# Kernel optimization log

Hardware: AMD Instinct MI355X
Metric: run time of the kernel (lower is better)

The kernel has to match this reference:

```python
import jax, jax.numpy as jnp
import numpy as np

N = 500000   # active voxels
CIN = 32
COUT = 64
K = 27       # 3x3x3 kernel taps
G = 8        # group norm groups
EPS = 1e-5


def group_norm(x, gamma, beta, num_groups=G, eps=EPS):
    # fvnn GroupNorm on sparse features with batch size 1: normalize each
    # channel-group over all active voxels (spatial) and channels in group.
    n, c = x.shape
    xg = x.reshape(n, num_groups, c // num_groups)
    mean = xg.mean(axis=(0, 2), keepdims=True)
    var = xg.var(axis=(0, 2), keepdims=True)
    xn = ((xg - mean) * jax.lax.rsqrt(var + eps)).reshape(n, c)
    return xn * gamma + beta


def sparse_conv(x, nbr_idx, W):
    # gather-based sparse 3x3x3 conv: W is [K, Cin, Cout]; loop over the 27
    # fixed kernel taps to avoid materializing the full [N, K, Cin] gather.
    out = jnp.zeros((x.shape[0], W.shape[2]), x.dtype)
    for k in range(W.shape[0]):
        out = out + jnp.take(x, nbr_idx[:, k], axis=0) @ W[k]
    return out


def setup_inputs() -> dict:
    key = jax.random.key(0)
    ks = jax.random.split(key, 8)
    s1 = 1.0 / np.sqrt(K * CIN)
    s2 = 1.0 / np.sqrt(K * COUT)
    return {
        "x": jax.random.normal(ks[0], (N, CIN), jnp.float32),
        "nbr_idx": jax.random.randint(ks[1], (N, K), 0, N, jnp.int32),
        "gamma1": jnp.ones((CIN,), jnp.float32),
        "beta1": jnp.zeros((CIN,), jnp.float32),
        "W1": jax.random.normal(ks[2], (K, CIN, COUT), jnp.float32) * s1,
        "gamma2": jnp.ones((COUT,), jnp.float32),
        "beta2": jnp.zeros((COUT,), jnp.float32),
        "W2": jax.random.normal(ks[3], (K, COUT, COUT), jnp.float32) * s2,
        "Wskip": jax.random.normal(ks[4], (CIN, COUT), jnp.float32) * (1.0 / np.sqrt(CIN)),
        "bskip": jnp.zeros((COUT,), jnp.float32),
        "feat_depth": 0,
    }


def reference(x, nbr_idx, gamma1, beta1, W1, gamma2, beta2, W2, Wskip, bskip, feat_depth):
    # decoder SparseResBlock, order 'gcs': GN -> SparseConv(bias=False) -> SiLU
    h = jax.nn.silu(sparse_conv(group_norm(x, gamma1, beta1), nbr_idx, W1))
    h = jax.nn.silu(sparse_conv(group_norm(h, gamma2, beta2), nbr_idx, W2))
    skip = x @ Wskip + bskip  # 1x1 sparse conv == per-voxel linear
    return (h + skip, feat_depth)
```

## Files before the change

### kernel.cpp

```cpp
#include <hip/hip_runtime.h>
#include <hip/hip_bf16.h>

typedef __bf16 bf16x8 __attribute__((ext_vector_type(8)));
typedef __bf16 bf16x4 __attribute__((ext_vector_type(4)));
typedef float  f32x4  __attribute__((ext_vector_type(4)));

#define MFMA16(a, b, c) __builtin_amdgcn_mfma_f32_16x16x32_bf16((a), (b), (c), 0, 0, 0)

__global__ void zero_stats_kernel(float* s) { s[threadIdx.x] = 0.0f; }

__global__ __launch_bounds__(256) void caststats_kernel(
    const float4* __restrict__ x, bf16x4* __restrict__ xb,
    float* __restrict__ stats, int nvec)
{
    int nth = gridDim.x * blockDim.x;
    int gt = blockIdx.x * blockDim.x + threadIdx.x;
    float s = 0.f, ss = 0.f;
    for (int f = gt; f < nvec; f += nth) {
        float4 v = x[f];
        s  += v.x + v.y + v.z + v.w;
        ss += v.x * v.x + v.y * v.y + v.z * v.z + v.w * v.w;
        bf16x4 b;
        b[0] = (__bf16)v.x; b[1] = (__bf16)v.y;
        b[2] = (__bf16)v.z; b[3] = (__bf16)v.w;
        xb[f] = b;
    }
    __shared__ float ls[16];
    if (threadIdx.x < 16) ls[threadIdx.x] = 0.f;
    __syncthreads();
    int g = gt & 7;
    atomicAdd(&ls[2 * g], s);
    atomicAdd(&ls[2 * g + 1], ss);
    __syncthreads();
    if (threadIdx.x < 16) atomicAdd(&stats[threadIdx.x], ls[threadIdx.x]);
}

__global__ __launch_bounds__(256) void fold1_kernel(
    const float* __restrict__ W1, const float* __restrict__ gamma1,
    const float* __restrict__ beta1, const float* __restrict__ Wskip,
    const float* __restrict__ stats1,
    __bf16* __restrict__ bp1, __bf16* __restrict__ bps,
    float* __restrict__ bias1,
    const int* __restrict__ feat, int* __restrict__ feat_out, float inv_n)
{
    int b = blockIdx.x, t = threadIdx.x;
    if (b < 216) {
        int e = b * 256 + t;
        int j = e & 7, lane = (e >> 3) & 63, ct = (e >> 9) & 3, k = e >> 11;
        int ci = ((lane >> 4) << 3) + j;
        int co = (ct << 4) + (lane & 15);
        int g = ci >> 2;
        float mean = stats1[2 * g] * inv_n;
        float var  = stats1[2 * g + 1] * inv_n - mean * mean;
        float r = rsqrtf(var + 1e-5f);
        float a = gamma1[ci] * r;
        bp1[e] = (__bf16)(a * W1[k * 2048 + ci * 64 + co]);
    } else if (b == 216) {
        if (t < 64) {
            float sum = 0.0f;
            for (int ci = 0; ci < 32; ++ci) {
                int g = ci >> 2;
                float mean = stats1[2 * g] * inv_n;
                float var  = stats1[2 * g + 1] * inv_n - mean * mean;
                float r = rsqrtf(var + 1e-5f);
                float a = gamma1[ci] * r;
                float bb = beta1[ci] - mean * a;
                float ws = 0.0f;
                for (int k = 0; k < 27; ++k) ws += W1[k * 2048 + ci * 64 + t];
                sum += bb * ws;
            }
            bias1[t] = sum;
        } else if (t == 64) {
            feat_out[0] = feat[0];
        }
    } else {
        int e = (b - 217) * 256 + t;
        int j = e & 7, lane = (e >> 3) & 63, ct = e >> 9;
        int ci = ((lane >> 4) << 3) + j;
        int co = (ct << 4) + (lane & 15);
        bps[e] = (__bf16)Wskip[ci * 64 + co];
    }
}

__global__ __launch_bounds__(256) void fold2_kernel(
    const float* __restrict__ W2, const float* __restrict__ gamma2,
    const float* __restrict__ beta2, const float* __restrict__ stats2,
    __bf16* __restrict__ bp2, float* __restrict__ bias2, float inv_n)
{
    int b = blockIdx.x, t = threadIdx.x;
    if (b < 432) {
        int e = b * 256 + t;
        int j = e & 7, lane = (e >> 3) & 63, ct = (e >> 9) & 3, hf = (e >> 11) & 1, k = e >> 12;
        int ci = (hf << 5) + ((lane >> 4) << 3) + j;
        int co = (ct << 4) + (lane & 15);
        int g = ci >> 3;
        float mean = stats2[2 * g] * inv_n;
        float var  = stats2[2 * g + 1] * inv_n - mean * mean;
        float r = rsqrtf(var + 1e-5f);
        float a = gamma2[ci] * r;
        bp2[e] = (__bf16)(a * W2[k * 4096 + ci * 64 + co]);
    } else if (t < 64) {
        float sum = 0.0f;
        for (int ci = 0; ci < 64; ++ci) {
            int g = ci >> 3;
            float mean = stats2[2 * g] * inv_n;
            float var  = stats2[2 * g + 1] * inv_n - mean * mean;
            float r = rsqrtf(var + 1e-5f);
            float a = gamma2[ci] * r;
            float bb = beta2[ci] - mean * a;
            float ws = 0.0f;
            for (int k = 0; k < 27; ++k) ws += W2[k * 4096 + ci * 64 + t];
            sum += bb * ws;
        }
        bias2[t] = sum;
    }
}

__global__ __launch_bounds__(256) void conv1_kernel(
    const __bf16* __restrict__ xb, const int* __restrict__ nbr,
    const __bf16* __restrict__ bp1, const float* __restrict__ bias1,
    __bf16* __restrict__ h, float* __restrict__ stats2, int N)
{
    __shared__ int sidx[4][27 * 16];
    __shared__ float ls[16];
    const int wav = threadIdx.x >> 6, lane = threadIdx.x & 63;
    const int v0 = (blockIdx.x * 4 + wav) * 16;
    const bool act = v0 < N;
    if (threadIdx.x < 16) ls[threadIdx.x] = 0.f;
    const int lm = lane & 15, q = lane >> 4;
    f32x4 acc0 = {0.f,0.f,0.f,0.f}, acc1 = acc0, acc2 = acc0, acc3 = acc0;
    if (act) {
        const int* gi = nbr + (size_t)v0 * 27;
        for (int i = lane; i < 432; i += 64) sidx[wav][i] = gi[i];
        const bf16x8* __restrict__ bpv = (const bf16x8*)bp1;
        for (int k = 0; k < 27; ++k) {
            int nb = sidx[wav][lm * 27 + k];
            bf16x8 a = *(const bf16x8*)(xb + (size_t)nb * 32 + q * 8);
            int bb = k * 256 + lane;
            acc0 = MFMA16(a, bpv[bb],       acc0);
            acc1 = MFMA16(a, bpv[bb + 64],  acc1);
            acc2 = MFMA16(a, bpv[bb + 128], acc2);
            acc3 = MFMA16(a, bpv[bb + 192], acc3);
        }
    }
    __syncthreads();
    if (act) {
#define EPI1(ACC, CT) { \
        float bsv = bias1[(CT) * 16 + lm]; \
        float ps = 0.f, pss = 0.f; \
        _Pragma("unroll") \
        for (int r = 0; r < 4; ++r) { \
            float val = ACC[r] + bsv; \
            val = val / (1.0f + __expf(-val)); \
            h[(size_t)(v0 + q * 4 + r) * 64 + (CT) * 16 + lm] = (__bf16)val; \
            ps += val; pss += val * val; } \
        int g2 = (CT) * 2 + (lm >> 3); \
        atomicAdd(&ls[2 * g2], ps); atomicAdd(&ls[2 * g2 + 1], pss); }
        EPI1(acc0, 0) EPI1(acc1, 1) EPI1(acc2, 2) EPI1(acc3, 3)
#undef EPI1
    }
    __syncthreads();
    if (threadIdx.x < 16) atomicAdd(&stats2[threadIdx.x], ls[threadIdx.x]);
}

__global__ __launch_bounds__(256) void conv2_kernel(
    const __bf16* __restrict__ h, const __bf16* __restrict__ xb,
    const int* __restrict__ nbr,
    const __bf16* __restrict__ bp2, const __bf16* __restrict__ bps,
    const float* __restrict__ bias2, const float* __restrict__ bskip,
    float* __restrict__ out, int N)
{
    __shared__ int sidx[4][27 * 16];
    const int wav = threadIdx.x >> 6, lane = threadIdx.x & 63;
    const int v0 = (blockIdx.x * 4 + wav) * 16;
    if (v0 >= N) return;
    const int* gi = nbr + (size_t)v0 * 27;
    for (int i = lane; i < 432; i += 64) sidx[wav][i] = gi[i];
    const int lm = lane & 15, q = lane >> 4;
    f32x4 c0 = {0.f,0.f,0.f,0.f}, c1 = c0, c2 = c0, c3 = c0;
    f32x4 s0 = c0, s1 = c0, s2 = c0, s3 = c0;
    const bf16x8* __restrict__ bpv = (const bf16x8*)bp2;
    const bf16x8* __restrict__ bsp = (const bf16x8*)bps;
    {
        bf16x8 ax = *(const bf16x8*)(xb + (size_t)(v0 + lm) * 32 + q * 8);
        s0 = MFMA16(ax, bsp[lane],       s0);
        s1 = MFMA16(ax, bsp[64 + lane],  s1);
        s2 = MFMA16(ax, bsp[128 + lane], s2);
        s3 = MFMA16(ax, bsp[192 + lane], s3);
    }
    for (int k = 0; k < 27; ++k) {
        int nb = sidx[wav][lm * 27 + k];
        const __bf16* hr = h + (size_t)nb * 64;
        bf16x8 a0 = *(const bf16x8*)(hr + q * 8);
        bf16x8 a1 = *(const bf16x8*)(hr + 32 + q * 8);
        int bb = k * 512 + lane;
        c0 = MFMA16(a0, bpv[bb],       c0);
        c1 = MFMA16(a0, bpv[bb + 64],  c1);
        c2 = MFMA16(a0, bpv[bb + 128], c2);
        c3 = MFMA16(a0, bpv[bb + 192], c3);
        c0 = MFMA16(a1, bpv[bb + 256], c0);
        c1 = MFMA16(a1, bpv[bb + 320], c1);
        c2 = MFMA16(a1, bpv[bb + 384], c2);
        c3 = MFMA16(a1, bpv[bb + 448], c3);
    }
#define EPI2(CC, SS, CT) { \
        int co = (CT) * 16 + lm; \
        float b2v = bias2[co]; \
        float bsk = bskip[co]; \
        _Pragma("unroll") \
        for (int r = 0; r < 4; ++r) { \
            float val = CC[r] + b2v; \
            val = val / (1.0f + __expf(-val)); \
            val += SS[r] + bsk; \
            out[(size_t)(v0 + q * 4 + r) * 64 + co] = val; } }
    EPI2(c0, s0, 0) EPI2(c1, s1, 1) EPI2(c2, s2, 2) EPI2(c3, s3, 3)
#undef EPI2
}

extern "C" void kernel_launch(void* const* d_in, const int* in_sizes, int n_in,
                              void* d_out, int out_size, void* d_ws, size_t ws_size,
                              hipStream_t stream)
{
    (void)n_in; (void)out_size; (void)ws_size;
    const float* x      = (const float*)d_in[0];
    const int*   nbr    = (const int*)d_in[1];
    const float* gamma1 = (const float*)d_in[2];
    const float* beta1  = (const float*)d_in[3];
    const float* W1     = (const float*)d_in[4];
    const float* gamma2 = (const float*)d_in[5];
    const float* beta2  = (const float*)d_in[6];
    const float* W2     = (const float*)d_in[7];
    const float* Wskip  = (const float*)d_in[8];
    const float* bskip  = (const float*)d_in[9];
    const int*   feat   = (const int*)d_in[10];
    const int N = in_sizes[0] / 32;

    char* ws = (char*)d_ws;
    float* stats1 = (float*)ws;
    float* stats2 = stats1 + 16;
    float* bias1  = stats1 + 32;
    float* bias2  = stats1 + 96;
    __bf16* bp1 = (__bf16*)(ws + (1 << 10));
    __bf16* bps = (__bf16*)(ws + (1 << 17));
    __bf16* bp2 = (__bf16*)(ws + 144 * 1024);
    __bf16* xb  = (__bf16*)(ws + (1 << 20));
    __bf16* h   = (__bf16*)(ws + (size_t)34 * (1 << 20));
    float* outb = (float*)d_out;

    const int convBlocks = (N / 16 + 3) / 4;

    hipLaunchKernelGGL(zero_stats_kernel, dim3(1), dim3(32), 0, stream, stats1);
    hipLaunchKernelGGL(caststats_kernel, dim3(2048), dim3(256), 0, stream,
                       (const float4*)x, (bf16x4*)xb, stats1, N * 8);
    hipLaunchKernelGGL(fold1_kernel, dim3(225), dim3(256), 0, stream,
                       W1, gamma1, beta1, Wskip, stats1, bp1, bps, bias1,
                       feat, (int*)(outb + (size_t)N * 64),
                       1.0f / (4.0f * (float)N));
    hipLaunchKernelGGL(conv1_kernel, dim3(convBlocks), dim3(256), 0, stream,
                       xb, nbr, bp1, bias1, h, stats2, N);
    hipLaunchKernelGGL(fold2_kernel, dim3(433), dim3(256), 0, stream,
                       W2, gamma2, beta2, stats2, bp2, bias2,
                       1.0f / (8.0f * (float)N));
    hipLaunchKernelGGL(conv2_kernel, dim3(convBlocks), dim3(256), 0, stream,
                       h, xb, nbr, bp2, bps, bias2, bskip, outb, N);
}
```

Before: 928.8 us.

## Process two voxel tiles per wave with prefetched gathers in sparse convs

```diff
diff --git a/kernel.cpp b/kernel.cpp
--- a/kernel.cpp
+++ b/kernel.cpp
@@ -116,104 +116,170 @@
     }
 }
 
-__global__ __launch_bounds__(256) void conv1_kernel(
+__global__ __launch_bounds__(256, 4) void conv1_kernel(
     const __bf16* __restrict__ xb, const int* __restrict__ nbr,
     const __bf16* __restrict__ bp1, const float* __restrict__ bias1,
-    __bf16* __restrict__ h, float* __restrict__ stats2, int N)
-{
-    __shared__ int sidx[4][27 * 16];
+    __bf16* __restrict__ h, float* __restrict__ stats2, int nTiles)
+{
+    __shared__ int sidx[4][864];
     __shared__ float ls[16];
     const int wav = threadIdx.x >> 6, lane = threadIdx.x & 63;
-    const int v0 = (blockIdx.x * 4 + wav) * 16;
-    const bool act = v0 < N;
+    const int unit = blockIdx.x * 4 + wav;
+    const int t0 = unit * 2;
+    const bool act0 = t0 < nTiles, act1 = t0 + 1 < nTiles;
     if (threadIdx.x < 16) ls[threadIdx.x] = 0.f;
     const int lm = lane & 15, q = lane >> 4;
-    f32x4 acc0 = {0.f,0.f,0.f,0.f}, acc1 = acc0, acc2 = acc0, acc3 = acc0;
-    if (act) {
-        const int* gi = nbr + (size_t)v0 * 27;
-        for (int i = lane; i < 432; i += 64) sidx[wav][i] = gi[i];
+    f32x4 c[8] = {};
+    if (act0) {
+        const int* gi = nbr + (size_t)t0 * 432;
+        const int cnt = act1 ? 864 : 432;
+        for (int i = lane; i < 864; i += 64) sidx[wav][i] = (i < cnt) ? gi[i] : 0;
+        const int* s0p = &sidx[wav][lm * 27];
+        const int* s1p = &sidx[wav][432 + lm * 27];
         const bf16x8* __restrict__ bpv = (const bf16x8*)bp1;
+        bf16x8 a0 = *(const bf16x8*)(xb + (size_t)s0p[0] * 32 + q * 8);
+        bf16x8 a1 = *(const bf16x8*)(xb + (size_t)s1p[0] * 32 + q * 8);
+#pragma unroll
         for (int k = 0; k < 27; ++k) {
-            int nb = sidx[wav][lm * 27 + k];
-            bf16x8 a = *(const bf16x8*)(xb + (size_t)nb * 32 + q * 8);
+            bf16x8 n0 = a0, n1 = a1;
+            if (k < 26) {
+                n0 = *(const bf16x8*)(xb + (size_t)s0p[k + 1] * 32 + q * 8);
+                n1 = *(const bf16x8*)(xb + (size_t)s1p[k + 1] * 32 + q * 8);
+            }
             int bb = k * 256 + lane;
-            acc0 = MFMA16(a, bpv[bb],       acc0);
-            acc1 = MFMA16(a, bpv[bb + 64],  acc1);
-            acc2 = MFMA16(a, bpv[bb + 128], acc2);
-            acc3 = MFMA16(a, bpv[bb + 192], acc3);
+            bf16x8 b0 = bpv[bb], b1 = bpv[bb + 64], b2 = bpv[bb + 128], b3 = bpv[bb + 192];
+            c[0] = MFMA16(a0, b0, c[0]);
+            c[1] = MFMA16(a0, b1, c[1]);
+            c[2] = MFMA16(a0, b2, c[2]);
+            c[3] = MFMA16(a0, b3, c[3]);
+            c[4] = MFMA16(a1, b0, c[4]);
+            c[5] = MFMA16(a1, b1, c[5]);
+            c[6] = MFMA16(a1, b2, c[6]);
+            c[7] = MFMA16(a1, b3, c[7]);
+            a0 = n0; a1 = n1;
         }
     }
     __syncthreads();
-    if (act) {
-#define EPI1(ACC, CT) { \
+    if (act0) {
+#define EPI1(CI, CT, V0) { \
         float bsv = bias1[(CT) * 16 + lm]; \
         float ps = 0.f, pss = 0.f; \
         _Pragma("unroll") \
         for (int r = 0; r < 4; ++r) { \
-            float val = ACC[r] + bsv; \
+            float val = c[CI][r] + bsv; \
             val = val / (1.0f + __expf(-val)); \
-            h[(size_t)(v0 + q * 4 + r) * 64 + (CT) * 16 + lm] = (__bf16)val; \
+            h[(size_t)((V0) + q * 4 + r) * 64 + (CT) * 16 + lm] = (__bf16)val; \
             ps += val; pss += val * val; } \
         int g2 = (CT) * 2 + (lm >> 3); \
         atomicAdd(&ls[2 * g2], ps); atomicAdd(&ls[2 * g2 + 1], pss); }
-        EPI1(acc0, 0) EPI1(acc1, 1) EPI1(acc2, 2) EPI1(acc3, 3)
+        const int v0 = t0 * 16;
+        EPI1(0, 0, v0) EPI1(1, 1, v0) EPI1(2, 2, v0) EPI1(3, 3, v0)
+        if (act1) {
+            const int v1 = v0 + 16;
+            EPI1(4, 0, v1) EPI1(5, 1, v1) EPI1(6, 2, v1) EPI1(7, 3, v1)
+        }
 #undef EPI1
     }
     __syncthreads();
     if (threadIdx.x < 16) atomicAdd(&stats2[threadIdx.x], ls[threadIdx.x]);
 }
 
-__global__ __launch_bounds__(256) void conv2_kernel(
+__global__ __launch_bounds__(256, 4) void conv2_kernel(
     const __bf16* __restrict__ h, const __bf16* __restrict__ xb,
     const int* __restrict__ nbr,
     const __bf16* __restrict__ bp2, const __bf16* __restrict__ bps,
     const float* __restrict__ bias2, const float* __restrict__ bskip,
-    float* __restrict__ out, int N)
-{
-    __shared__ int sidx[4][27 * 16];
+    float* __restrict__ out, int nTiles)
+{
+    __shared__ int sidx[4][864];
     const int wav = threadIdx.x >> 6, lane = threadIdx.x & 63;
-    const int v0 = (blockIdx.x * 4 + wav) * 16;
-    if (v0 >= N) return;
-    const int* gi = nbr + (size_t)v0 * 27;
-    for (int i = lane; i < 432; i += 64) sidx[wav][i] = gi[i];
+    const int unit = blockIdx.x * 4 + wav;
+    const int t0 = unit * 2;
+    const bool act0 = t0 < nTiles, act1 = t0 + 1 < nTiles;
+    if (!act0) return;
     const int lm = lane & 15, q = lane >> 4;
-    f32x4 c0 = {0.f,0.f,0.f,0.f}, c1 = c0, c2 = c0, c3 = c0;
-    f32x4 s0 = c0, s1 = c0, s2 = c0, s3 = c0;
+    const int* gi = nbr + (size_t)t0 * 432;
+    const int cnt = act1 ? 864 : 432;
+    for (int i = lane; i < 864; i += 64) sidx[wav][i] = (i < cnt) ? gi[i] : 0;
+    const int* s0p = &sidx[wav][lm * 27];
+    const int* s1p = &sidx[wav][432 + lm * 27];
     const bf16x8* __restrict__ bpv = (const bf16x8*)bp2;
     const bf16x8* __restrict__ bsp = (const bf16x8*)bps;
+    f32x4 c[8] = {};
     {
-        bf16x8 ax = *(const bf16x8*)(xb + (size_t)(v0 + lm) * 32 + q * 8);
-        s0 = MFMA16(ax, bsp[lane],       s0);
-        s1 = MFMA16(ax, bsp[64 + lane],  s1);
-        s2 = MFMA16(ax, bsp[128 + lane], s2);
-        s3 = MFMA16(ax, bsp[192 + lane], s3);
-    }
-    for (int k = 0; k < 27; ++k) {
-        int nb = sidx[wav][lm * 27 + k];
-        const __bf16* hr = h + (size_t)nb * 64;
-        bf16x8 a0 = *(const bf16x8*)(hr + q * 8);
-        bf16x8 a1 = *(const bf16x8*)(hr + 32 + q * 8);
-        int bb = k * 512 + lane;
-        c0 = MFMA16(a0, bpv[bb],       c0);
-        c1 = MFMA16(a0, bpv[bb + 64],  c1);
-        c2 = MFMA16(a0, bpv[bb + 128], c2);
-        c3 = MFMA16(a0, bpv[bb + 192], c3);
-        c0 = MFMA16(a1, bpv[bb + 256], c0);
-        c1 = MFMA16(a1, bpv[bb + 320], c1);
-        c2 = MFMA16(a1, bpv[bb + 384], c2);
-        c3 = MFMA16(a1, bpv[bb + 448], c3);
-    }
-#define EPI2(CC, SS, CT) { \
+        const __bf16* r0 = h + (size_t)s0p[0] * 64;
+        const __bf16* r1 = h + (size_t)s1p[0] * 64;
+        bf16x8 a0l = *(const bf16x8*)(r0 + q * 8);
+        bf16x8 a0h = *(const bf16x8*)(r0 + 32 + q * 8);
+        bf16x8 a1l = *(const bf16x8*)(r1 + q * 8);
+        bf16x8 a1h = *(const bf16x8*)(r1 + 32 + q * 8);
+#pragma unroll
+        for (int k = 0; k < 27; ++k) {
+            bf16x8 n0l = a0l, n0h = a0h, n1l = a1l, n1h = a1h;
+            if (k < 26) {
+                const __bf16* p0 = h + (size_t)s0p[k + 1] * 64;
+                const __bf16* p1 = h + (size_t)s1p[k + 1] * 64;
+                n0l = *(const bf16x8*)(p0 + q * 8);
+                n0h = *(const bf16x8*)(p0 + 32 + q * 8);
+                n1l = *(const bf16x8*)(p1 + q * 8);
+                n1h = *(const bf16x8*)(p1 + 32 + q * 8);
+            }
+            int bb = k * 512 + lane;
+            bf16x8 b0 = bpv[bb],       b1 = bpv[bb + 64];
+            bf16x8 b2 = bpv[bb + 128], b3 = bpv[bb + 192];
+            c[0] = MFMA16(a0l, b0, c[0]);
+            c[1] = MFMA16(a0l, b1, c[1]);
+            c[2] = MFMA16(a0l, b2, c[2]);
+            c[3] = MFMA16(a0l, b3, c[3]);
+            c[4] = MFMA16(a1l, b0, c[4]);
+            c[5] = MFMA16(a1l, b1, c[5]);
+            c[6] = MFMA16(a1l, b2, c[6]);
+            c[7] = MFMA16(a1l, b3, c[7]);
+            bf16x8 b4 = bpv[bb + 256], b5 = bpv[bb + 320];
+            bf16x8 b6 = bpv[bb + 384], b7 = bpv[bb + 448];
+            c[0] = MFMA16(a0h, b4, c[0]);
+            c[1] = MFMA16(a0h, b5, c[1]);
+            c[2] = MFMA16(a0h, b6, c[2]);
+            c[3] = MFMA16(a0h, b7, c[3]);
+            c[4] = MFMA16(a1h, b4, c[4]);
+            c[5] = MFMA16(a1h, b5, c[5]);
+            c[6] = MFMA16(a1h, b6, c[6]);
+            c[7] = MFMA16(a1h, b7, c[7]);
+            a0l = n0l; a0h = n0h; a1l = n1l; a1h = n1h;
+        }
+    }
+    f32x4 s[8] = {};
+    {
+        bf16x8 ax0 = *(const bf16x8*)(xb + ((size_t)t0 * 16 + lm) * 32 + q * 8);
+        bf16x8 w0 = bsp[lane], w1 = bsp[64 + lane], w2 = bsp[128 + lane], w3 = bsp[192 + lane];
+        s[0] = MFMA16(ax0, w0, s[0]);
+        s[1] = MFMA16(ax0, w1, s[1]);
+        s[2] = MFMA16(ax0, w2, s[2]);
+        s[3] = MFMA16(ax0, w3, s[3]);
+        if (act1) {
+            bf16x8 ax1 = *(const bf16x8*)(xb + ((size_t)t0 * 16 + 16 + lm) * 32 + q * 8);
+            s[4] = MFMA16(ax1, w0, s[4]);
+            s[5] = MFMA16(ax1, w1, s[5]);
+            s[6] = MFMA16(ax1, w2, s[6]);
+            s[7] = MFMA16(ax1, w3, s[7]);
+        }
+    }
+#define EPI2(CI, CT, V0) { \
         int co = (CT) * 16 + lm; \
         float b2v = bias2[co]; \
         float bsk = bskip[co]; \
         _Pragma("unroll") \
         for (int r = 0; r < 4; ++r) { \
-            float val = CC[r] + b2v; \
+            float val = c[CI][r] + b2v; \
             val = val / (1.0f + __expf(-val)); \
-            val += SS[r] + bsk; \
-            out[(size_t)(v0 + q * 4 + r) * 64 + co] = val; } }
-    EPI2(c0, s0, 0) EPI2(c1, s1, 1) EPI2(c2, s2, 2) EPI2(c3, s3, 3)
+            val += s[CI][r] + bsk; \
+            out[(size_t)((V0) + q * 4 + r) * 64 + co] = val; } }
+    const int v0 = t0 * 16;
+    EPI2(0, 0, v0) EPI2(1, 1, v0) EPI2(2, 2, v0) EPI2(3, 3, v0)
+    if (act1) {
+        const int v1 = v0 + 16;
+        EPI2(4, 0, v1) EPI2(5, 1, v1) EPI2(6, 2, v1) EPI2(7, 3, v1)
+    }
 #undef EPI2
 }
 
@@ -247,7 +313,9 @@
     __bf16* h   = (__bf16*)(ws + (size_t)34 * (1 << 20));
     float* outb = (float*)d_out;
 
-    const int convBlocks = (N / 16 + 3) / 4;
+    const int nTiles = (N + 15) / 16;
+    const int units = (nTiles + 1) / 2;
+    const int convBlocks = (units + 3) / 4;
 
     hipLaunchKernelGGL(zero_stats_kernel, dim3(1), dim3(32), 0, stream, stats1);
     hipLaunchKernelGGL(caststats_kernel, dim3(2048), dim3(256), 0, stream,
@@ -257,10 +325,10 @@
                        feat, (int*)(outb + (size_t)N * 64),
                        1.0f / (4.0f * (float)N));
     hipLaunchKernelGGL(conv1_kernel, dim3(convBlocks), dim3(256), 0, stream,
-                       xb, nbr, bp1, bias1, h, stats2, N);
+                       xb, nbr, bp1, bias1, h, stats2, nTiles);
     hipLaunchKernelGGL(fold2_kernel, dim3(433), dim3(256), 0, stream,
                        W2, gamma2, beta2, stats2, bp2, bias2,
                        1.0f / (8.0f * (float)N));
     hipLaunchKernelGGL(conv2_kernel, dim3(convBlocks), dim3(256), 0, stream,
-                       h, xb, nbr, bp2, bps, bias2, bskip, outb, N);
-}
+                       h, xb, nbr, bp2, bps, bias2, bskip, outb, nTiles);
+}
```

Measured after the change: 864.3 us. 1.07x faster.
